# Performance work log

Hardware: AMD Instinct MI355X
Metric: run time of the kernel (lower is better)

Reference implementation:

```python
import jax, jax.numpy as jnp
import numpy as np

V_DECAY = float(np.exp(-1.0 / 100.0))   # voltage_tau = 100
S_DECAY = float(np.exp(-1.0 / 50.0))    # synapse_tau = 50
THRESH = 1.0                            # spiking_threshold

N_IN = 8192
N_OUT = 8192


def setup_inputs() -> dict:
    key = jax.random.key(0)
    k1, k2, k3, k4 = jax.random.split(key, 4)
    input_spikes = jax.random.uniform(k1, (N_IN,), dtype=jnp.float32)
    voltages = jax.random.normal(k2, (1, N_OUT), dtype=jnp.float32)
    synapses = jax.random.normal(k3, (N_IN, N_OUT), dtype=jnp.float32)
    weights = jax.random.normal(k4, (N_IN, N_OUT), dtype=jnp.float32)
    return {"input_spikes": input_spikes, "voltages": voltages,
            "synapses": synapses, "weights": weights}


def reference(input_spikes, voltages, synapses, weights):
    # voltages *= voltage_decay
    v = voltages * V_DECAY                              # [1, n_out]
    # output_spikes = voltages >= threshold (computed on decayed voltage)
    spikes = v >= THRESH                                # [1, n_out] bool
    # synapses *= synapse_decay; per-column loop == rank-1 broadcast add
    syn = synapses * S_DECAY + weights * input_spikes[:, None]  # [n_in, n_out]
    # voltages += synapses.sum(dim=0) - spikes * threshold
    v_new = v + syn.sum(axis=0) - spikes.astype(v.dtype) * THRESH  # [1, n_out]
    return spikes, v_new, syn
```

## Files before the change

### kernel.cpp

```cpp
#include <hip/hip_runtime.h>


#define V_DECAY 0.99004983374916811f
#define S_DECAY 0.98019867330675525f
#define THRESH  1.0f

constexpr int N_IN  = 8192;
constexpr int N_OUT = 8192;
constexpr int STEPS = 8;

typedef float f32x4 __attribute__((ext_vector_type(4)));

__global__ __launch_bounds__(256) void lif_syn_kernel(
    const float* __restrict__ input_spikes,
    const float* __restrict__ synapses,
    const float* __restrict__ weights,
    float* __restrict__ syn_out,
    float* __restrict__ partials,
    int rowsPerBlock)
{
    const int rc   = blockIdx.x;
    const int row0 = rc * rowsPerBlock;
    const int c0   = threadIdx.x * 4;

    f32x4 acc[STEPS];
    #pragma unroll
    for (int s = 0; s < STEPS; ++s) acc[s] = (f32x4)(0.f);

    for (int r = 0; r < rowsPerBlock; ++r) {
        const float  sp   = input_spikes[row0 + r];
        const size_t base = (size_t)(row0 + r) * N_OUT + c0;
        f32x4 sv[STEPS], wv[STEPS];
        #pragma unroll
        for (int s = 0; s < STEPS; ++s) {
            sv[s] = *reinterpret_cast<const f32x4*>(synapses + base + s * 1024);
            wv[s] = *reinterpret_cast<const f32x4*>(weights  + base + s * 1024);
        }
        __builtin_amdgcn_sched_barrier(0);
        #pragma unroll
        for (int s = 0; s < STEPS; ++s) {
            const f32x4 o = sv[s] * S_DECAY + wv[s] * sp;
            *reinterpret_cast<f32x4*>(syn_out + base + s * 1024) = o;
            acc[s] += o;
        }
    }
    const size_t pbase = (size_t)rc * N_OUT + c0;
    #pragma unroll
    for (int s = 0; s < STEPS; ++s)
        *reinterpret_cast<f32x4*>(partials + pbase + s * 1024) = acc[s];
}

__global__ __launch_bounds__(256) void lif_reduce_kernel(
    float* __restrict__ partials)
{
    const int ctiles = N_OUT / 256;
    const int c = (blockIdx.x % ctiles) * 256 + threadIdx.x;
    const int g = blockIdx.x / ctiles;
    float sum = 0.f;
    #pragma unroll
    for (int k = 0; k < 16; ++k)
        sum += partials[(size_t)(g * 16 + k) * N_OUT + c];
    partials[(size_t)(g * 16) * N_OUT + c] = sum;
}

__global__ __launch_bounds__(256) void lif_v_kernel(
    const float* __restrict__ voltages,
    const float* __restrict__ partials,
    float* __restrict__ out,
    int nGroups, int rowStride)
{
    const int c = blockIdx.x * blockDim.x + threadIdx.x;
    const float v     = voltages[c] * V_DECAY;
    const float spike = (v >= THRESH) ? 1.0f : 0.0f;
    float sum = 0.f;
    #pragma unroll 8
    for (int g = 0; g < nGroups; ++g)
        sum += partials[(size_t)(g * rowStride) * N_OUT + c];
    out[c]         = spike;
    out[N_OUT + c] = v + sum - spike * THRESH;
}

extern "C" void kernel_launch(void* const* d_in, const int* in_sizes, int n_in,
                              void* d_out, int out_size, void* d_ws, size_t ws_size,
                              hipStream_t stream) {
    const float* input_spikes = (const float*)d_in[0];
    const float* voltages     = (const float*)d_in[1];
    const float* synapses     = (const float*)d_in[2];
    const float* weights      = (const float*)d_in[3];

    float* out      = (float*)d_out;
    float* syn_out  = out + 2 * N_OUT;
    float* partials = (float*)d_ws;

    int chunks = 512;
    while (chunks > 1 && (size_t)chunks * N_OUT * sizeof(float) > ws_size)
        chunks >>= 1;
    const int rowsPerBlock = N_IN / chunks;

    lif_syn_kernel<<<dim3(chunks), dim3(256), 0, stream>>>(
        input_spikes, synapses, weights, syn_out, partials, rowsPerBlock);

    if (chunks >= 16) {
        lif_reduce_kernel<<<dim3((N_OUT / 256) * (chunks / 16)), dim3(256), 0,
                            stream>>>(partials);
        lif_v_kernel<<<dim3(N_OUT / 256), dim3(256), 0, stream>>>(
            voltages, partials, out, chunks / 16, 16);
    } else {
        lif_v_kernel<<<dim3(N_OUT / 256), dim3(256), 0, stream>>>(
            voltages, partials, out, chunks, 1);
    }
}
```

Measured before the change: 167.6 us.

## Split columns across two blocks and double-buffer row loads in syn kernel

```diff
diff --git a/kernel.cpp b/kernel.cpp
--- a/kernel.cpp
+++ b/kernel.cpp
@@ -7,47 +7,81 @@
 
 constexpr int N_IN  = 8192;
 constexpr int N_OUT = 8192;
-constexpr int STEPS = 8;
+constexpr int HALF  = 4096;
 
 typedef float f32x4 __attribute__((ext_vector_type(4)));
 
-__global__ __launch_bounds__(256) void lif_syn_kernel(
+#define DECL_SET(P) f32x4 P##s0, P##s1, P##s2, P##s3, P##w0, P##w1, P##w2, P##w3; float P##sp;
+
+#define LOAD_SET(P, ROW) do {                                        \
+    const size_t b_ = (size_t)(ROW) * N_OUT + c0;                    \
+    P##s0 = *(const f32x4*)(synapses + b_);                          \
+    P##s1 = *(const f32x4*)(synapses + b_ + 1024);                   \
+    P##s2 = *(const f32x4*)(synapses + b_ + 2048);                   \
+    P##s3 = *(const f32x4*)(synapses + b_ + 3072);                   \
+    P##w0 = *(const f32x4*)(weights  + b_);                          \
+    P##w1 = *(const f32x4*)(weights  + b_ + 1024);                   \
+    P##w2 = *(const f32x4*)(weights  + b_ + 2048);                   \
+    P##w3 = *(const f32x4*)(weights  + b_ + 3072);                   \
+    P##sp = input_spikes[ROW];                                       \
+} while (0)
+
+#define PIN_SET(P)                                                   \
+    asm volatile("" : "+v"(P##s0), "+v"(P##s1), "+v"(P##s2), "+v"(P##s3), \
+                      "+v"(P##w0), "+v"(P##w1), "+v"(P##w2), "+v"(P##w3))
+
+#define COMP_SET(P, ROW) do {                                        \
+    const size_t b_ = (size_t)(ROW) * N_OUT + c0;                    \
+    const f32x4 o0 = P##s0 * S_DECAY + P##w0 * P##sp;                \
+    const f32x4 o1 = P##s1 * S_DECAY + P##w1 * P##sp;                \
+    const f32x4 o2 = P##s2 * S_DECAY + P##w2 * P##sp;                \
+    const f32x4 o3 = P##s3 * S_DECAY + P##w3 * P##sp;                \
+    *(f32x4*)(syn_out + b_)        = o0;                             \
+    *(f32x4*)(syn_out + b_ + 1024) = o1;                             \
+    *(f32x4*)(syn_out + b_ + 2048) = o2;                             \
+    *(f32x4*)(syn_out + b_ + 3072) = o3;                             \
+    acc0 += o0; acc1 += o1; acc2 += o2; acc3 += o3;                  \
+} while (0)
+
+__global__ __launch_bounds__(256, 4) void lif_syn_kernel(
     const float* __restrict__ input_spikes,
     const float* __restrict__ synapses,
     const float* __restrict__ weights,
     float* __restrict__ syn_out,
     float* __restrict__ partials,
-    int rowsPerBlock)
+    int rowsPerChunk)
 {
-    const int rc   = blockIdx.x;
-    const int row0 = rc * rowsPerBlock;
-    const int c0   = threadIdx.x * 4;
+    const int h    = blockIdx.x & 1;
+    const int rc   = blockIdx.x >> 1;
+    const int c0   = h * HALF + threadIdx.x * 4;
+    const int row0 = rc * rowsPerChunk;
 
-    f32x4 acc[STEPS];
-    #pragma unroll
-    for (int s = 0; s < STEPS; ++s) acc[s] = (f32x4)(0.f);
+    f32x4 acc0 = (f32x4)(0.f), acc1 = (f32x4)(0.f),
+          acc2 = (f32x4)(0.f), acc3 = (f32x4)(0.f);
 
-    for (int r = 0; r < rowsPerBlock; ++r) {
-        const float  sp   = input_spikes[row0 + r];
-        const size_t base = (size_t)(row0 + r) * N_OUT + c0;
-        f32x4 sv[STEPS], wv[STEPS];
+    DECL_SET(A); DECL_SET(B);
+
+    for (int rr = 0; rr < rowsPerChunk; rr += 16) {
+        const int rbase = row0 + rr;
+        LOAD_SET(A, rbase);
         #pragma unroll
-        for (int s = 0; s < STEPS; ++s) {
-            sv[s] = *reinterpret_cast<const f32x4*>(synapses + base + s * 1024);
-            wv[s] = *reinterpret_cast<const f32x4*>(weights  + base + s * 1024);
-        }
-        __builtin_amdgcn_sched_barrier(0);
-        #pragma unroll
-        for (int s = 0; s < STEPS; ++s) {
-            const f32x4 o = sv[s] * S_DECAY + wv[s] * sp;
-            *reinterpret_cast<f32x4*>(syn_out + base + s * 1024) = o;
-            acc[s] += o;
+        for (int r = 0; r < 16; r += 2) {
+            LOAD_SET(B, rbase + r + 1);
+            __builtin_amdgcn_sched_barrier(0);
+            PIN_SET(A);
+            COMP_SET(A, rbase + r);
+            if (r + 2 < 16) LOAD_SET(A, rbase + r + 2);
+            __builtin_amdgcn_sched_barrier(0);
+            PIN_SET(B);
+            COMP_SET(B, rbase + r + 1);
         }
     }
+
     const size_t pbase = (size_t)rc * N_OUT + c0;
-    #pragma unroll
-    for (int s = 0; s < STEPS; ++s)
-        *reinterpret_cast<f32x4*>(partials + pbase + s * 1024) = acc[s];
+    *(f32x4*)(partials + pbase)        = acc0;
+    *(f32x4*)(partials + pbase + 1024) = acc1;
+    *(f32x4*)(partials + pbase + 2048) = acc2;
+    *(f32x4*)(partials + pbase + 3072) = acc3;
 }
 
 __global__ __launch_bounds__(256) void lif_reduce_kernel(
@@ -95,10 +129,10 @@
     int chunks = 512;
     while (chunks > 1 && (size_t)chunks * N_OUT * sizeof(float) > ws_size)
         chunks >>= 1;
-    const int rowsPerBlock = N_IN / chunks;
+    const int rowsPerChunk = N_IN / chunks;
 
-    lif_syn_kernel<<<dim3(chunks), dim3(256), 0, stream>>>(
-        input_spikes, synapses, weights, syn_out, partials, rowsPerBlock);
+    lif_syn_kernel<<<dim3(2 * chunks), dim3(256), 0, stream>>>(
+        input_spikes, synapses, weights, syn_out, partials, rowsPerChunk);
 
     if (chunks >= 16) {
         lif_reduce_kernel<<<dim3((N_OUT / 256) * (chunks / 16)), dim3(256), 0,
```

Result: no change. 165.4 us (median of 2 runs) (-1.3%).
